# Optimization experiments

Measured on AMD Instinct MI355X. Metric: run time of the kernel, lower is better.

Reference implementation:

```python
import jax, jax.numpy as jnp
import numpy as np

EPS = 1e-5
B, CIN, L = 512, 5, 1024   # batch, input channels, msp length == d_model
COUT, A, NB = 32, 13, 5    # CNN branch channels, max_atoms, num_bonds_prediction


def conv1d(x, w, pad, groups=1):
    # x: (N, C, L), w: (O, I/groups, K)
    return jax.lax.conv_general_dilated(
        x, w, window_strides=(1,), padding=[(pad, pad)],
        dimension_numbers=("NCH", "OIH", "NCH"), feature_group_count=groups)


def batchnorm(x, g, b):
    # training-mode BN over (N, L) per channel, as nn.BatchNorm1d in train()
    m = jnp.mean(x, axis=(0, 2), keepdims=True)
    v = jnp.var(x, axis=(0, 2), keepdims=True)
    return (x - m) * jax.lax.rsqrt(v + EPS) * g[None, :, None] + b[None, :, None]


def setup_inputs() -> dict:
    key = jax.random.key(0)
    ks = jax.random.split(key, 16)
    n = jax.random.normal
    inp = {
        "src": n(ks[0], (B, CIN, L), dtype=jnp.float32),
        "mask": jnp.ones((B, A), dtype=bool),
        "max_atoms": A,
        # CNN branch 1 (kernel 5) : depthwise, pointwise, BN, residual 1x1 conv
        "dw1": n(ks[1], (CIN, 1, 5), dtype=jnp.float32) * 0.2,
        "pw1": n(ks[2], (COUT, CIN, 1), dtype=jnp.float32) * 0.2,
        "g1": jnp.ones((COUT,), jnp.float32),
        "be1": jnp.zeros((COUT,), jnp.float32),
        "r1w": n(ks[3], (COUT, CIN, 1), dtype=jnp.float32) * 0.2,
        "r1b": jnp.zeros((COUT,), jnp.float32),
        # CNN branch 2 (kernel 3)
        "dw2": n(ks[4], (CIN, 1, 3), dtype=jnp.float32) * 0.2,
        "pw2": n(ks[5], (COUT, CIN, 1), dtype=jnp.float32) * 0.2,
        "g2": jnp.ones((COUT,), jnp.float32),
        "be2": jnp.zeros((COUT,), jnp.float32),
        "r2w": n(ks[6], (COUT, CIN, 1), dtype=jnp.float32) * 0.2,
        "r2b": jnp.zeros((COUT,), jnp.float32),
        # EdgeClassify2 linears: ll1 (2*COUT -> A), fl (2*L -> NB)
        "ll1w": n(ks[7], (A, 2 * COUT), dtype=jnp.float32) * 0.1,
        "ll1b": jnp.zeros((A,), jnp.float32),
        "flw": n(ks[8], (NB, 2 * L), dtype=jnp.float32) * 0.02,
        "flb": jnp.zeros((NB,), jnp.float32),
    }
    return inp


def reference(src, mask, max_atoms, dw1, pw1, g1, be1, r1w, r1b,
              dw2, pw2, g2, be2, r2w, r2b, ll1w, ll1b, flw, flb):
    # ---- CNN encoder ----
    e1 = jax.nn.relu(batchnorm(conv1d(conv1d(src, dw1, 2, groups=CIN), pw1, 0), g1, be1))
    e1 = e1 * (conv1d(src, r1w, 0) + r1b[None, :, None])
    e2 = jax.nn.relu(batchnorm(conv1d(conv1d(src, dw2, 1, groups=CIN), pw2, 0), g2, be2))
    e2 = e2 * (conv1d(src, r2w, 0) + r2b[None, :, None])
    x = jnp.concatenate([e1, e2], axis=1)          # (B, 2*COUT, L)
    # ---- EdgeClassify2 ----
    # ll1 over channel dim: (B, 2*COUT, L) -> (B, A, L)
    h = jnp.einsum("bcl,ac->bal", x, ll1w) + ll1b[None, :, None]
    # vectorized replacement of the O(A^2) python loop:
    # final_e[:, i, j] = concat(h[:, min(i,j)], h[:, max(i,j)])
    idx = jnp.arange(max_atoms)
    mn = jnp.minimum(idx[:, None], idx[None, :])   # (A, A)
    mx = jnp.maximum(idx[:, None], idx[None, :])
    final_e = jnp.concatenate([h[:, mn, :], h[:, mx, :]], axis=-1)  # (B, A, A, 2L)
    out = jnp.einsum("bijd,nd->bijn", final_e, flw) + flb           # (B, A, A, NB)
    return out
```

## Files before the change

### kernel.cpp

```cpp
#include <hip/hip_runtime.h>
#include <hip/hip_bf16.h>

#define BB 512
#define LL 1024
#define AA 13
#define NBP 5
#define NTOT (BB * LL)
#define EPSV 1e-5f

#define WS_F     192
#define WS_PART  256
#define WS_CONST 10496
#define WS_FLW   16384

typedef __attribute__((ext_vector_type(8))) short bhalf8;
typedef __attribute__((ext_vector_type(4))) float floatx4;

__device__ __forceinline__ void trunc_pair(float e0, float e1, unsigned int& hp, unsigned int& lp) {
    unsigned int u0 = __float_as_uint(e0), u1 = __float_as_uint(e1);
    unsigned int h0 = u0 & 0xFFFF0000u, h1 = u1 & 0xFFFF0000u;
    hp = (h0 >> 16) | h1;
    float l0 = e0 - __uint_as_float(h0);
    float l1 = e1 - __uint_as_float(h1);
    lp = (__float_as_uint(l0) >> 16) | (__float_as_uint(l1) & 0xFFFF0000u);
}

template<int CTRL, int RM, bool BC>
__device__ __forceinline__ float dppadd(float v) {
    int t = __builtin_amdgcn_update_dpp(0, __float_as_int(v), CTRL, RM, 0xf, BC);
    return v + __int_as_float(t);
}
__device__ __forceinline__ float wave_sum(float v) {
    v = dppadd<0x111, 0xf, true >(v);
    v = dppadd<0x112, 0xf, true >(v);
    v = dppadd<0x114, 0xf, true >(v);
    v = dppadd<0x118, 0xf, true >(v);
    v = dppadd<0x142, 0xa, false>(v);
    v = dppadd<0x143, 0xc, false>(v);
    return v;
}

__global__ __launch_bounds__(256) void k_moments(
    const float* __restrict__ src,
    const float* __restrict__ dw1,
    const float* __restrict__ dw2,
    const float* __restrict__ flw,
    float* __restrict__ ws)
{
    __shared__ float red[4][40];
    __shared__ float fred[4];
    int tid = threadIdx.x;
    int gid = blockIdx.x * 256 + tid;
    int b = gid >> 7, L0 = (gid & 127) << 3;
    const float* sb = src + b * (5 * LL);

    float w1[5][5], w2[5][3];
#pragma unroll
    for (int c = 0; c < 5; c++) {
#pragma unroll
        for (int t = 0; t < 5; t++) w1[c][t] = dw1[c*5+t];
#pragma unroll
        for (int t = 0; t < 3; t++) w2[c][t] = dw2[c*3+t];
    }

    float x[5][16];
#pragma unroll
    for (int c5 = 0; c5 < 5; c5++) {
        const float* sp = sb + c5 * LL;
        float4 xa = (L0 >= 4)    ? *(const float4*)(sp + L0 - 4) : make_float4(0,0,0,0);
        float4 xb = *(const float4*)(sp + L0);
        float4 xc = *(const float4*)(sp + L0 + 4);
        float4 xd = (L0 <= 1012) ? *(const float4*)(sp + L0 + 8) : make_float4(0,0,0,0);
        x[c5][0]=xa.x; x[c5][1]=xa.y; x[c5][2]=xa.z; x[c5][3]=xa.w;
        x[c5][4]=xb.x; x[c5][5]=xb.y; x[c5][6]=xb.z; x[c5][7]=xb.w;
        x[c5][8]=xc.x; x[c5][9]=xc.y; x[c5][10]=xc.z; x[c5][11]=xc.w;
        x[c5][12]=xd.x; x[c5][13]=xd.y; x[c5][14]=xd.z; x[c5][15]=xd.w;
    }

    float acc[40];
#pragma unroll
    for (int k = 0; k < 40; k++) acc[k] = 0.f;

#pragma unroll
    for (int k = 0; k < 8; k++) {
        float d1[5], d2[5];
#pragma unroll
        for (int c5 = 0; c5 < 5; c5++) {
            d1[c5] = w1[c5][0]*x[c5][k+2] + w1[c5][1]*x[c5][k+3] + w1[c5][2]*x[c5][k+4]
                   + w1[c5][3]*x[c5][k+5] + w1[c5][4]*x[c5][k+6];
            d2[c5] = w2[c5][0]*x[c5][k+3] + w2[c5][1]*x[c5][k+4] + w2[c5][2]*x[c5][k+5];
        }
#pragma unroll
        for (int j = 0; j < 5; j++) { acc[j] += d1[j]; acc[20+j] += d2[j]; }
#pragma unroll
        for (int j = 0; j < 5; j++)
#pragma unroll
            for (int kk = j; kk < 5; kk++) {
                int idx = j*(11-j)/2 + (kk - j);
                acc[5+idx]  += d1[j]*d1[kk];
                acc[25+idx] += d2[j]*d2[kk];
            }
    }

    int lane = tid & 63, wv = tid >> 6;
#pragma unroll
    for (int k = 0; k < 40; k++) acc[k] = wave_sum(acc[k]);
    if (lane == 63) {
#pragma unroll
        for (int k = 0; k < 40; k++) red[wv][k] = acc[k];
    }
    __syncthreads();
    if (tid < 40) {
        ws[WS_PART + blockIdx.x * 40 + tid] =
            red[0][tid] + red[1][tid] + red[2][tid] + red[3][tid];
    }

    if (blockIdx.x < 10) {
        int nn = blockIdx.x;
        int n = nn < 5 ? nn : nn - 5;
        int off = nn < 5 ? 0 : LL;
        float4 v = *(const float4*)(flw + n * (2*LL) + off + tid * 4);
        {
            unsigned int hp0, lp0, hp1, lp1;
            trunc_pair(v.x, v.y, hp0, lp0);
            trunc_pair(v.z, v.w, hp1, lp1);
            char* fwb = (char*)(ws + WS_FLW);
            *(uint2*)(fwb + nn * 2048 + tid * 8)         = make_uint2(hp0, hp1);
            *(uint2*)(fwb + 32768 + nn * 2048 + tid * 8) = make_uint2(lp0, lp1);
        }
        float s = wave_sum(v.x + v.y + v.z + v.w);
        if (lane == 63) fred[wv] = s;
        __syncthreads();
        if (tid == 0) ws[WS_F + nn] = fred[0] + fred[1] + fred[2] + fred[3];
    } else if (blockIdx.x < 16) {
        int nn = blockIdx.x;
        char* fwb = (char*)(ws + WS_FLW);
        *(uint2*)(fwb + nn * 2048 + tid * 8)         = make_uint2(0u, 0u);
        *(uint2*)(fwb + 32768 + nn * 2048 + tid * 8) = make_uint2(0u, 0u);
    }
}

__global__ __launch_bounds__(320) void k_prep(
    float* __restrict__ ws,
    const float* __restrict__ pw1, const float* __restrict__ pw2,
    const float* __restrict__ g1,  const float* __restrict__ be1,
    const float* __restrict__ g2,  const float* __restrict__ be2,
    const float* __restrict__ r1w, const float* __restrict__ r2w,
    const float* __restrict__ r1b, const float* __restrict__ r2b)
{
    __shared__ float momS[40];
    int tid = threadIdx.x;
    {
        int k = tid >> 3, sub = tid & 7;
        float v = 0.f;
#pragma unroll 8
        for (int t2 = 0; t2 < 32; t2++) v += ws[WS_PART + (sub + (t2 << 3)) * 40 + k];
        v += __shfl_xor(v, 1, 64);
        v += __shfl_xor(v, 2, 64);
        v += __shfl_xor(v, 4, 64);
        if (sub == 0) momS[k] = v;
    }
    __syncthreads();
    if (tid < 64) {
        int brc = tid >> 5, o = tid & 31;
        const float invN = 1.0f / (float)NTOT;
        const float* pw = brc ? pw2 : pw1;
        const float* rw = brc ? r2w : r1w;
        const float* s  = momS + (brc ? 20 : 0);
        const float* M  = momS + (brc ? 25 : 5);
        float pwv[5], rwv[5], md[5];
#pragma unroll
        for (int j = 0; j < 5; j++) { pwv[j] = pw[o*5+j]; rwv[j] = rw[o*5+j]; md[j] = s[j] * invN; }
        float meanY = 0.f;
#pragma unroll
        for (int j = 0; j < 5; j++) meanY += pwv[j] * md[j];
        float ey2 = 0.f;
#pragma unroll
        for (int j = 0; j < 5; j++)
#pragma unroll
            for (int k = 0; k < 5; k++) {
                int lo = j < k ? j : k, hi = j < k ? k : j;
                int idx = lo*(11-lo)/2 + (hi - lo);
                ey2 += pwv[j] * pwv[k] * (M[idx] * invN);
            }
        float varY = ey2 - meanY * meanY;
        if (varY < 0.f) varY = 0.f;
        float gg = brc ? g2[o] : g1[o];
        float bb = brc ? be2[o] : be1[o];
        float rb = brc ? r2b[o] : r1b[o];
        float sc = gg * rsqrtf(varY + EPSV);
        float sh = bb - meanY * sc;
        float* dst = ws + WS_CONST + tid * 16;
        dst[0] = pwv[0]*sc; dst[1] = pwv[1]*sc; dst[2] = pwv[2]*sc; dst[3] = pwv[3]*sc;
        dst[4] = pwv[4]*sc; dst[5] = sh;        dst[6] = rb;        dst[7] = 0.f;
        dst[8] = rwv[0];    dst[9] = rwv[1];    dst[10] = rwv[2];   dst[11] = rwv[3];
        dst[12] = rwv[4];   dst[13] = 0.f;      dst[14] = 0.f;      dst[15] = 0.f;
    }
}

__device__ __forceinline__ float e_val(const float4& A, const float4& B2, const float4& R0, float r4w,
                                       const float4& pa, const float4& pb, float svx, float svy) {
    float y = B2.y + A.x*pa.x + A.y*pa.y + A.z*pa.z + A.w*pa.w + B2.x*pb.x;
    float r = B2.z + R0.x*pb.y + R0.y*pb.z + R0.z*pb.w + R0.w*svx + r4w*svy;
    return fmaxf(y, 0.f) * r;
}

__global__ __launch_bounds__(512, 2) void k_fused(
    const float* __restrict__ src,
    const float* __restrict__ dw1,
    const float* __restrict__ dw2,
    const float* __restrict__ ll1w,
    const float* __restrict__ ll1b,
    const float* __restrict__ flb,
    const float* __restrict__ ws_ro,
    float* __restrict__ out)
{
    __shared__ __align__(16) float dvS[18432];
    __shared__ float llT[832];
    __shared__ float PQ[130];

    int tid = threadIdx.x, b = blockIdx.x;
    int lane = tid & 63;
    int gu = __builtin_amdgcn_readfirstlane(tid >> 6);
    int mp = gu >> 2;
    int lq = gu & 3;
    int row = lane & 15;
    int ko = lane >> 4;

    const float* srcB = src + b * (5 * LL);
    char* base  = (char*)dvS;
    char* cbase = (char*)(dvS + 16384);

    for (int t = tid; t < 1024; t += 512) {
        int swz = ((t >> 3) & 3) << 4;
        float d1v[5], d2v[5], s0[5];
#pragma unroll
        for (int c5 = 0; c5 < 5; c5++) {
            const float* s5 = srcB + (c5 << 10);
            float xm2 = (t >= 2)    ? s5[t - 2] : 0.f;
            float xm1 = (t >= 1)    ? s5[t - 1] : 0.f;
            float x0  = s5[t];
            float xp1 = (t <= 1022) ? s5[t + 1] : 0.f;
            float xp2 = (t <= 1021) ? s5[t + 2] : 0.f;
            d1v[c5] = dw1[c5*5+0]*xm2 + dw1[c5*5+1]*xm1 + dw1[c5*5+2]*x0
                    + dw1[c5*5+3]*xp1 + dw1[c5*5+4]*xp2;
            d2v[c5] = dw2[c5*3+0]*xm1 + dw2[c5*3+1]*x0 + dw2[c5*3+2]*xp1;
            s0[c5] = x0;
        }
        *(float4*)(base + ((((0<<11)+(t<<1)+0) << 4) ^ swz)) = make_float4(d1v[0],d1v[1],d1v[2],d1v[3]);
        *(float4*)(base + ((((0<<11)+(t<<1)+1) << 4) ^ swz)) = make_float4(d1v[4],s0[0],s0[1],s0[2]);
        *(float4*)(base + ((((1<<11)+(t<<1)+0) << 4) ^ swz)) = make_float4(d2v[0],d2v[1],d2v[2],d2v[3]);
        *(float4*)(base + ((((1<<11)+(t<<1)+1) << 4) ^ swz)) = make_float4(d2v[4],s0[0],s0[1],s0[2]);
        *(float2*)(cbase + (t << 3)) = make_float2(s0[3], s0[4]);
    }
    for (int idx = tid; idx < 832; idx += 512) {
        int cc = idx / 13, a = idx - cc * 13;
        llT[idx] = ll1w[a * 64 + cc];
    }
    __syncthreads();

    int chA = (mp << 5) + row;
    int chB = chA + 16;
    const float* cfA = ws_ro + WS_CONST + (chA << 4);
    const float4 Aa = *(const float4*)cfA;
    const float4 Ba = *(const float4*)(cfA + 4);
    const float4 Ra = *(const float4*)(cfA + 8);
    const float  a4 = cfA[12];
    const float* cfB = ws_ro + WS_CONST + (chB << 4);
    const float4 Ab = *(const float4*)cfB;
    const float4 Bb = *(const float4*)(cfB + 4);
    const float4 Rb = *(const float4*)(cfB + 8);
    const float  b4 = cfB[12];

    const char* fwb = (const char*)(ws_ro + WS_FLW);
    floatx4 CA = {0.f, 0.f, 0.f, 0.f};
    floatx4 CB = {0.f, 0.f, 0.f, 0.f};

#pragma unroll 1
    for (int s = 0; s < 8; ++s) {
        int kstep = (lq << 3) + s;
        int l0 = (kstep << 5) + (ko << 3);
        union { uint4 u; bhalf8 v; } bh, bl;
        {
            int boff = ((row << 10) + l0) << 1;
            bh.u = *(const uint4*)(fwb + boff);
            bl.u = *(const uint4*)(fwb + 32768 + boff);
        }
        int sw = ((l0 >> 3) & 3) << 4;
        int ebase = (mp << 15) + (l0 << 5);
        union { unsigned int u[4]; bhalf8 v; } ahA, alA, ahB, alB;
#pragma unroll
        for (int jp = 0; jp < 4; ++jp) {
            int o0 = ebase + (jp << 6);
            const float4 pa0 = *(const float4*)(base + ((o0      ) ^ sw));
            const float4 pb0 = *(const float4*)(base + ((o0 + 16) ^ sw));
            const float4 pa1 = *(const float4*)(base + ((o0 + 32) ^ sw));
            const float4 pb1 = *(const float4*)(base + ((o0 + 48) ^ sw));
            const float4 pcc = *(const float4*)(cbase + ((l0 + (jp << 1)) << 3));
            float e0 = e_val(Aa, Ba, Ra, a4, pa0, pb0, pcc.x, pcc.y);
            float e1 = e_val(Aa, Ba, Ra, a4, pa1, pb1, pcc.z, pcc.w);
            trunc_pair(e0, e1, ahA.u[jp], alA.u[jp]);
            float f0 = e_val(Ab, Bb, Rb, b4, pa0, pb0, pcc.x, pcc.y);
            float f1 = e_val(Ab, Bb, Rb, b4, pa1, pb1, pcc.z, pcc.w);
            trunc_pair(f0, f1, ahB.u[jp], alB.u[jp]);
        }
        CA = __builtin_amdgcn_mfma_f32_16x16x32_bf16(ahA.v, bh.v, CA, 0, 0, 0);
        CA = __builtin_amdgcn_mfma_f32_16x16x32_bf16(ahA.v, bl.v, CA, 0, 0, 0);
        CA = __builtin_amdgcn_mfma_f32_16x16x32_bf16(alA.v, bh.v, CA, 0, 0, 0);
        CB = __builtin_amdgcn_mfma_f32_16x16x32_bf16(ahB.v, bh.v, CB, 0, 0, 0);
        CB = __builtin_amdgcn_mfma_f32_16x16x32_bf16(ahB.v, bl.v, CB, 0, 0, 0);
        CB = __builtin_amdgcn_mfma_f32_16x16x32_bf16(alB.v, bh.v, CB, 0, 0, 0);
    }

    __syncthreads();
    {
        float* part = dvS;
        int basep = ((lane >> 4) << 6) + (lane & 15);
        int sA = (gu << 1) * 256, sB = sA + 256;
        part[sA + basep]      = CA[0];
        part[sA + basep + 16] = CA[1];
        part[sA + basep + 32] = CA[2];
        part[sA + basep + 48] = CA[3];
        part[sB + basep]      = CB[0];
        part[sB + basep + 16] = CB[1];
        part[sB + basep + 32] = CB[2];
        part[sB + basep + 48] = CB[3];
    }
    __syncthreads();
    float* SarrF = dvS + 4096;
    for (int idx = tid; idx < 1024; idx += 512) {
        int c = idx >> 4, n = idx & 15;
        int mt2 = c >> 4, m = c & 15;
        int mp2 = mt2 >> 1, t2 = mt2 & 1;
        const float* part = (const float*)dvS;
        int o = (m << 4) + n;
        float sum = 0.f;
#pragma unroll
        for (int lq2 = 0; lq2 < 4; ++lq2)
            sum += part[((((mp2 << 2) + lq2) << 1) + t2) * 256 + o];
        SarrF[idx] = sum;
    }
    __syncthreads();

    if (tid < 130) {
        int half = tid >= 65 ? 1 : 0;
        int q = tid - half * 65;
        int a = q / 5, n = q - a * 5;
        int col = half * 5 + n;
        float v = ll1b[a] * ws_ro[WS_F + col];
#pragma unroll 8
        for (int cc = 0; cc < 64; cc++) v += llT[cc * 13 + a] * SarrF[(cc << 4) + col];
        PQ[tid] = v;
    }
    __syncthreads();

    for (int idx = tid; idx < AA * AA * NBP; idx += 512) {
        int i = idx / 65;
        int rr = idx - i * 65;
        int j = rr / 5, n = rr - j * 5;
        int mn = i < j ? i : j, mx = i < j ? j : i;
        out[b * (AA * AA * NBP) + idx] = PQ[mn * 5 + n] + PQ[65 + mx * 5 + n] + flb[n];
    }
}

extern "C" void kernel_launch(void* const* d_in, const int* in_sizes, int n_in,
                              void* d_out, int out_size, void* d_ws, size_t ws_size,
                              hipStream_t stream) {
    const float* src  = (const float*)d_in[0];
    const float* dw1  = (const float*)d_in[3];
    const float* pw1  = (const float*)d_in[4];
    const float* g1   = (const float*)d_in[5];
    const float* be1  = (const float*)d_in[6];
    const float* r1w  = (const float*)d_in[7];
    const float* r1b  = (const float*)d_in[8];
    const float* dw2  = (const float*)d_in[9];
    const float* pw2  = (const float*)d_in[10];
    const float* g2   = (const float*)d_in[11];
    const float* be2  = (const float*)d_in[12];
    const float* r2w  = (const float*)d_in[13];
    const float* r2b  = (const float*)d_in[14];
    const float* ll1w = (const float*)d_in[15];
    const float* ll1b = (const float*)d_in[16];
    const float* flw  = (const float*)d_in[17];
    const float* flb  = (const float*)d_in[18];
    float* ws  = (float*)d_ws;
    float* out = (float*)d_out;

    k_moments<<<256, 256, 0, stream>>>(src, dw1, dw2, flw, ws);
    k_prep<<<1, 320, 0, stream>>>(ws, pw1, pw2, g1, be1, g2, be2, r1w, r2w, r1b, r2b);
    k_fused<<<BB, 512, 0, stream>>>(src, dw1, dw2, ll1w, ll1b, flb, ws, out);
}
```

Before: 130.1 us.

## Split fused kernel across L halves and move output epilogue to separate kernel

Each batch element is now handled by two workgroups, one per half of the sequence length, which halves shared memory per block. The launch bound is raised so more blocks can be resident per CU. Partial projection sums are written to workspace and combined by a new small k_out kernel, which applies the ll1 projection and expands the pairwise output. This should improve occupancy and parallelism, at the cost of an extra kernel launch, a global round-trip for the partials, and duplicated per-block setup loads.

```diff
diff --git a/kernel.cpp b/kernel.cpp
--- a/kernel.cpp
+++ b/kernel.cpp
@@ -12,6 +12,7 @@
 #define WS_PART  256
 #define WS_CONST 10496
 #define WS_FLW   16384
+#define WS_S     40960
 
 typedef __attribute__((ext_vector_type(8))) short bhalf8;
 typedef __attribute__((ext_vector_type(4))) float floatx4;
@@ -38,6 +39,13 @@
     v = dppadd<0x142, 0xa, false>(v);
     v = dppadd<0x143, 0xc, false>(v);
     return v;
+}
+
+__device__ __forceinline__ float e_val(const float4& A, const float4& B2, const float4& R0, float r4w,
+                                       const float4& pa, const float4& pb, float svx, float svy) {
+    float y = B2.y + A.x*pa.x + A.y*pa.y + A.z*pa.z + A.w*pa.w + B2.x*pb.x;
+    float r = B2.z + R0.x*pb.y + R0.y*pb.z + R0.z*pb.w + R0.w*svx + r4w*svy;
+    return fmaxf(y, 0.f) * r;
 }
 
 __global__ __launch_bounds__(256) void k_moments(
@@ -198,28 +206,17 @@
     }
 }
 
-__device__ __forceinline__ float e_val(const float4& A, const float4& B2, const float4& R0, float r4w,
-                                       const float4& pa, const float4& pb, float svx, float svy) {
-    float y = B2.y + A.x*pa.x + A.y*pa.y + A.z*pa.z + A.w*pa.w + B2.x*pb.x;
-    float r = B2.z + R0.x*pb.y + R0.y*pb.z + R0.z*pb.w + R0.w*svx + r4w*svy;
-    return fmaxf(y, 0.f) * r;
-}
-
-__global__ __launch_bounds__(512, 2) void k_fused(
+__global__ __launch_bounds__(512, 4) void k_fused(
     const float* __restrict__ src,
     const float* __restrict__ dw1,
     const float* __restrict__ dw2,
-    const float* __restrict__ ll1w,
-    const float* __restrict__ ll1b,
-    const float* __restrict__ flb,
     const float* __restrict__ ws_ro,
-    float* __restrict__ out)
+    float* __restrict__ ws)
 {
-    __shared__ __align__(16) float dvS[18432];
-    __shared__ float llT[832];
-    __shared__ float PQ[130];
-
-    int tid = threadIdx.x, b = blockIdx.x;
+    __shared__ __align__(16) float dvS[9216];
+
+    int tid = threadIdx.x, bb = blockIdx.x;
+    int b = bb >> 1, h = bb & 1;
     int lane = tid & 63;
     int gu = __builtin_amdgcn_readfirstlane(tid >> 6);
     int mp = gu >> 2;
@@ -229,35 +226,7 @@
 
     const float* srcB = src + b * (5 * LL);
     char* base  = (char*)dvS;
-    char* cbase = (char*)(dvS + 16384);
-
-    for (int t = tid; t < 1024; t += 512) {
-        int swz = ((t >> 3) & 3) << 4;
-        float d1v[5], d2v[5], s0[5];
-#pragma unroll
-        for (int c5 = 0; c5 < 5; c5++) {
-            const float* s5 = srcB + (c5 << 10);
-            float xm2 = (t >= 2)    ? s5[t - 2] : 0.f;
-            float xm1 = (t >= 1)    ? s5[t - 1] : 0.f;
-            float x0  = s5[t];
-            float xp1 = (t <= 1022) ? s5[t + 1] : 0.f;
-            float xp2 = (t <= 1021) ? s5[t + 2] : 0.f;
-            d1v[c5] = dw1[c5*5+0]*xm2 + dw1[c5*5+1]*xm1 + dw1[c5*5+2]*x0
-                    + dw1[c5*5+3]*xp1 + dw1[c5*5+4]*xp2;
-            d2v[c5] = dw2[c5*3+0]*xm1 + dw2[c5*3+1]*x0 + dw2[c5*3+2]*xp1;
-            s0[c5] = x0;
-        }
-        *(float4*)(base + ((((0<<11)+(t<<1)+0) << 4) ^ swz)) = make_float4(d1v[0],d1v[1],d1v[2],d1v[3]);
-        *(float4*)(base + ((((0<<11)+(t<<1)+1) << 4) ^ swz)) = make_float4(d1v[4],s0[0],s0[1],s0[2]);
-        *(float4*)(base + ((((1<<11)+(t<<1)+0) << 4) ^ swz)) = make_float4(d2v[0],d2v[1],d2v[2],d2v[3]);
-        *(float4*)(base + ((((1<<11)+(t<<1)+1) << 4) ^ swz)) = make_float4(d2v[4],s0[0],s0[1],s0[2]);
-        *(float2*)(cbase + (t << 3)) = make_float2(s0[3], s0[4]);
-    }
-    for (int idx = tid; idx < 832; idx += 512) {
-        int cc = idx / 13, a = idx - cc * 13;
-        llT[idx] = ll1w[a * 64 + cc];
-    }
-    __syncthreads();
+    char* cbase = (char*)(dvS + 8192);
 
     int chA = (mp << 5) + row;
     int chB = chA + 16;
@@ -272,22 +241,47 @@
     const float4 Rb = *(const float4*)(cfB + 8);
     const float  b4 = cfB[12];
 
+    {
+        int t = tid, lg = (h << 9) + t;
+        int swz = ((t >> 3) & 3) << 4;
+        float d1v[5], d2v[5], s0[5];
+#pragma unroll
+        for (int c5 = 0; c5 < 5; c5++) {
+            const float* s5 = srcB + (c5 << 10);
+            float xm2 = (lg >= 2)    ? s5[lg - 2] : 0.f;
+            float xm1 = (lg >= 1)    ? s5[lg - 1] : 0.f;
+            float x0  = s5[lg];
+            float xp1 = (lg <= 1022) ? s5[lg + 1] : 0.f;
+            float xp2 = (lg <= 1021) ? s5[lg + 2] : 0.f;
+            d1v[c5] = dw1[c5*5+0]*xm2 + dw1[c5*5+1]*xm1 + dw1[c5*5+2]*x0
+                    + dw1[c5*5+3]*xp1 + dw1[c5*5+4]*xp2;
+            d2v[c5] = dw2[c5*3+0]*xm1 + dw2[c5*3+1]*x0 + dw2[c5*3+2]*xp1;
+            s0[c5] = x0;
+        }
+        *(float4*)(base + ((((0<<10)+(t<<1)+0) << 4) ^ swz)) = make_float4(d1v[0],d1v[1],d1v[2],d1v[3]);
+        *(float4*)(base + ((((0<<10)+(t<<1)+1) << 4) ^ swz)) = make_float4(d1v[4],s0[0],s0[1],s0[2]);
+        *(float4*)(base + ((((1<<10)+(t<<1)+0) << 4) ^ swz)) = make_float4(d2v[0],d2v[1],d2v[2],d2v[3]);
+        *(float4*)(base + ((((1<<10)+(t<<1)+1) << 4) ^ swz)) = make_float4(d2v[4],s0[0],s0[1],s0[2]);
+        *(float2*)(cbase + (t << 3)) = make_float2(s0[3], s0[4]);
+    }
+    __syncthreads();
+
     const char* fwb = (const char*)(ws_ro + WS_FLW);
     floatx4 CA = {0.f, 0.f, 0.f, 0.f};
     floatx4 CB = {0.f, 0.f, 0.f, 0.f};
 
 #pragma unroll 1
-    for (int s = 0; s < 8; ++s) {
-        int kstep = (lq << 3) + s;
+    for (int s = 0; s < 4; ++s) {
+        int kstep = (lq << 2) + s;
         int l0 = (kstep << 5) + (ko << 3);
         union { uint4 u; bhalf8 v; } bh, bl;
         {
-            int boff = ((row << 10) + l0) << 1;
+            int boff = ((row << 10) + (h << 9) + l0) << 1;
             bh.u = *(const uint4*)(fwb + boff);
             bl.u = *(const uint4*)(fwb + 32768 + boff);
         }
         int sw = ((l0 >> 3) & 3) << 4;
-        int ebase = (mp << 15) + (l0 << 5);
+        int ebase = (mp << 14) + (l0 << 5);
         union { unsigned int u[4]; bhalf8 v; } ahA, alA, ahB, alB;
 #pragma unroll
         for (int jp = 0; jp < 4; ++jp) {
@@ -327,9 +321,8 @@
         part[sB + basep + 48] = CB[3];
     }
     __syncthreads();
-    float* SarrF = dvS + 4096;
-    for (int idx = tid; idx < 1024; idx += 512) {
-        int c = idx >> 4, n = idx & 15;
+    for (int idx = tid; idx < 640; idx += 512) {
+        int c = idx / 10, n = idx - c * 10;
         int mt2 = c >> 4, m = c & 15;
         int mp2 = mt2 >> 1, t2 = mt2 & 1;
         const float* part = (const float*)dvS;
@@ -338,8 +331,29 @@
 #pragma unroll
         for (int lq2 = 0; lq2 < 4; ++lq2)
             sum += part[((((mp2 << 2) + lq2) << 1) + t2) * 256 + o];
-        SarrF[idx] = sum;
-    }
+        ws[WS_S + bb * 640 + idx] = sum;
+    }
+}
+
+__global__ __launch_bounds__(256) void k_out(
+    const float* __restrict__ ws,
+    const float* __restrict__ ll1w,
+    const float* __restrict__ ll1b,
+    const float* __restrict__ flb,
+    float* __restrict__ out)
+{
+    __shared__ float llT[832];
+    __shared__ float S[640];
+    __shared__ float PQ[130];
+
+    int tid = threadIdx.x, b = blockIdx.x;
+    for (int idx = tid; idx < 832; idx += 256) {
+        int cc = idx / 13, a = idx - cc * 13;
+        llT[idx] = ll1w[a * 64 + cc];
+    }
+    const float* s0 = ws + WS_S + (b * 2) * 640;
+    const float* s1 = ws + WS_S + (b * 2 + 1) * 640;
+    for (int idx = tid; idx < 640; idx += 256) S[idx] = s0[idx] + s1[idx];
     __syncthreads();
 
     if (tid < 130) {
@@ -347,14 +361,14 @@
         int q = tid - half * 65;
         int a = q / 5, n = q - a * 5;
         int col = half * 5 + n;
-        float v = ll1b[a] * ws_ro[WS_F + col];
+        float v = ll1b[a] * ws[WS_F + col];
 #pragma unroll 8
-        for (int cc = 0; cc < 64; cc++) v += llT[cc * 13 + a] * SarrF[(cc << 4) + col];
+        for (int cc = 0; cc < 64; cc++) v += llT[cc * 13 + a] * S[cc * 10 + col];
         PQ[tid] = v;
     }
     __syncthreads();
 
-    for (int idx = tid; idx < AA * AA * NBP; idx += 512) {
+    for (int idx = tid; idx < AA * AA * NBP; idx += 256) {
         int i = idx / 65;
         int rr = idx - i * 65;
         int j = rr / 5, n = rr - j * 5;
@@ -388,5 +402,6 @@
 
     k_moments<<<256, 256, 0, stream>>>(src, dw1, dw2, flw, ws);
     k_prep<<<1, 320, 0, stream>>>(ws, pw1, pw2, g1, be1, g2, be2, r1w, r2w, r1b, r2b);
-    k_fused<<<BB, 512, 0, stream>>>(src, dw1, dw2, ll1w, ll1b, flb, ws, out);
-}
+    k_fused<<<BB * 2, 512, 0, stream>>>(src, dw1, dw2, ws, ws);
+    k_out<<<BB, 256, 0, stream>>>(ws, ll1w, ll1b, flb, out);
+}
```

After: 132.9 us. 2.1% more time.
